# Optimization experiments

Hardware: AMD Instinct MI355X
Metric: run time of the kernel (lower is better)

## Reference

```python
import jax, jax.numpy as jnp
import numpy as np

N = 100000      # nodes
E = 1600000     # edges (avg degree 16)
IN, HID, OUT = 128, 32, 16
H = 2           # attention heads
EPS = 1e-5
NEG_SLOPE = 0.2


def setup_inputs() -> dict:
    key = jax.random.key(0)
    ks = jax.random.split(key, 24)
    f32 = jnp.float32
    def w(k, shape, scale=0.1):
        return jax.random.normal(k, shape, f32) * scale
    return {
        "x": jax.random.normal(ks[0], (N, IN), f32),
        "edge_index": jax.random.randint(ks[1], (2, E), 0, N, dtype=jnp.int32),
        # GCN layer 1
        "gcn1_W": w(ks[2], (IN, HID)), "gcn1_b": w(ks[3], (HID,)),
        # BN1 (eval mode: running stats)
        "bn1_g": 1.0 + w(ks[4], (HID,)), "bn1_b": w(ks[5], (HID,)),
        "bn1_m": w(ks[6], (HID,)), "bn1_v": 1.0 + jnp.abs(w(ks[7], (HID,))),
        # GAT layer 1 (HID -> HID, heads=H, concat=False)
        "gat1_W": w(ks[8], (HID, H * HID)), "gat1_as": w(ks[9], (H, HID)),
        "gat1_ad": w(ks[10], (H, HID)), "gat1_b": w(ks[11], (HID,)),
        # GCN layer 2
        "gcn2_W": w(ks[12], (HID, HID)), "gcn2_b": w(ks[13], (HID,)),
        # BN2
        "bn2_g": 1.0 + w(ks[14], (HID,)), "bn2_b": w(ks[15], (HID,)),
        "bn2_m": w(ks[16], (HID,)), "bn2_v": 1.0 + jnp.abs(w(ks[17], (HID,))),
        # GAT layer 2 (HID -> OUT, heads=H, concat=False)
        "gat2_W": w(ks[18], (HID, H * OUT)), "gat2_as": w(ks[19], (H, OUT)),
        "gat2_ad": w(ks[20], (H, OUT)), "gat2_b": w(ks[21], (OUT,)),
    }


def _add_self_loops(edge_index):
    loop = jnp.arange(N, dtype=edge_index.dtype)
    src = jnp.concatenate([edge_index[0], loop])
    dst = jnp.concatenate([edge_index[1], loop])
    return src, dst


def _gcn(x, src, dst, W, b):
    h = x @ W                                             # [N, F]
    deg = jax.ops.segment_sum(jnp.ones_like(dst, h.dtype), dst, N)
    dinv = jax.lax.rsqrt(jnp.maximum(deg, 1.0))
    norm = dinv[src] * dinv[dst]                          # [Etot]
    out = jax.ops.segment_sum(h[src] * norm[:, None], dst, N)
    return out + b


def _gat(x, src, dst, W, a_src, a_dst, b, F):
    # PyG GATConv (concat=False -> mean over heads); eval mode (no attn dropout)
    h = (x @ W).reshape(N, H, F)                          # [N, H, F]
    al_s = jnp.einsum('nhf,hf->nh', h, a_src)             # [N, H]
    al_d = jnp.einsum('nhf,hf->nh', h, a_dst)
    e = jax.nn.leaky_relu(al_s[src] + al_d[dst], NEG_SLOPE)  # [Etot, H]
    # segment softmax over destination neighborhoods (self-loops ensure >=1 edge)
    m = jax.ops.segment_max(e, dst, N)
    ex = jnp.exp(e - m[dst])
    s = jax.ops.segment_sum(ex, dst, N)
    alpha = ex / s[dst]                                   # [Etot, H]
    out = jax.ops.segment_sum(alpha[:, :, None] * h[src], dst, N)  # [N, H, F]
    return out.mean(axis=1) + b


def _bn_eval(x, g, b, m, v):
    return (x - m) * jax.lax.rsqrt(v + EPS) * g + b


def reference(x, edge_index, gcn1_W, gcn1_b, bn1_g, bn1_b, bn1_m, bn1_v,
              gat1_W, gat1_as, gat1_ad, gat1_b, gcn2_W, gcn2_b,
              bn2_g, bn2_b, bn2_m, bn2_v, gat2_W, gat2_as, gat2_ad, gat2_b):
    src, dst = _add_self_loops(edge_index)
    h = _gcn(x, src, dst, gcn1_W, gcn1_b)
    h = jax.nn.relu(_bn_eval(h, bn1_g, bn1_b, bn1_m, bn1_v))
    h = jax.nn.relu(_gat(h, src, dst, gat1_W, gat1_as, gat1_ad, gat1_b, HID))
    h = _gcn(h, src, dst, gcn2_W, gcn2_b)
    h = jax.nn.relu(_bn_eval(h, bn2_g, bn2_b, bn2_m, bn2_v))
    h = _gat(h, src, dst, gat2_W, gat2_as, gat2_ad, gat2_b, OUT)
    return jax.nn.log_softmax(h, axis=1)
```

## Files before the change

### kernel.cpp

```cpp
#include <hip/hip_runtime.h>
#include <hip/hip_bf16.h>

#define NN 100000
#define EE 1600000
#define SLAB 64
#define KB 391
#define CHUNK 4096

static constexpr float EPSV = 1e-5f;
static constexpr float SLOPE = 0.2f;

typedef unsigned short ushortt;

__device__ __forceinline__ float lrelu(float v) { return v > 0.f ? v : SLOPE * v; }

__device__ __forceinline__ unsigned rne_bf16(float v) {
    unsigned u = __float_as_uint(v);
    return (u + 0x7fffu + ((u >> 16) & 1u)) >> 16;
}
__device__ __forceinline__ float bf16_lo(unsigned u) { return __uint_as_float(u << 16); }
__device__ __forceinline__ float bf16_hi(unsigned u) { return __uint_as_float(u & 0xffff0000u); }
__device__ __forceinline__ float us2f(ushortt s) { return __uint_as_float((unsigned)s << 16); }


__global__ void k_z(int* __restrict__ hist) {
    int i = threadIdx.x;
    if (i < KB) hist[i] = 0;
}

__global__ __launch_bounds__(256) void k_hist(const int* __restrict__ dst, int* __restrict__ hist) {
    __shared__ int h[KB];
    int tid = threadIdx.x;
    for (int i = tid; i < KB; i += 256) h[i] = 0;
    __syncthreads();
    int e0 = blockIdx.x * CHUNK;
    #pragma unroll
    for (int r = 0; r < CHUNK / 256; ++r) {
        int e = e0 + r * 256 + tid;
        if (e < EE) atomicAdd(&h[dst[e] >> 8], 1);
    }
    __syncthreads();
    for (int i = tid; i < KB; i += 256)
        if (h[i]) atomicAdd(&hist[i], h[i]);
}

__global__ __launch_bounds__(512) void k_scan(const int* __restrict__ hist,
                                              int* __restrict__ start, int* __restrict__ gcur) {
    __shared__ int h[KB];
    int tid = threadIdx.x;
    for (int i = tid; i < KB; i += 512) h[i] = hist[i];
    __syncthreads();
    for (int t = tid; t < KB; t += 512) {
        int s = 0;
        for (int i = 0; i < t; ++i) s += h[i];
        start[t] = s;
        gcur[t] = 0;
    }
}

__global__ __launch_bounds__(256) void k_scat(const int* __restrict__ src, const int* __restrict__ dst,
                                              const int* __restrict__ start, int* __restrict__ gcur,
                                              unsigned int* __restrict__ ebuf) {
    __shared__ int hc[KB], hb[KB];
    int tid = threadIdx.x;
    for (int i = tid; i < KB; i += 256) hc[i] = 0;
    __syncthreads();
    int e0 = blockIdx.x * CHUNK;
    #pragma unroll
    for (int r = 0; r < CHUNK / 256; ++r) {
        int e = e0 + r * 256 + tid;
        if (e < EE) atomicAdd(&hc[dst[e] >> 8], 1);
    }
    __syncthreads();
    for (int i = tid; i < KB; i += 256) {
        int c = hc[i];
        if (c) hb[i] = atomicAdd(&gcur[i], c);
        hc[i] = 0;
    }
    __syncthreads();
    #pragma unroll
    for (int r = 0; r < CHUNK / 256; ++r) {
        int e = e0 + r * 256 + tid;
        if (e < EE) {
            int d = dst[e];
            int b = d >> 8;
            int rk = atomicAdd(&hc[b], 1);
            ebuf[start[b] + hb[b] + rk] = ((unsigned)src[e] << 8) | (unsigned)(d & 255);
        }
    }
}

__global__ __launch_bounds__(256) void k_bucket(const unsigned int* __restrict__ ebuf,
                                                const int* __restrict__ start, const int* __restrict__ hist,
                                                int* __restrict__ col, int* __restrict__ cnt) {
    __shared__ int lc[256];
    int tid = threadIdx.x;
    int b = blockIdx.x;
    lc[tid] = 0;
    __syncthreads();
    int s = start[b], nb = hist[b];
    for (int i = tid; i < nb; i += 256) {
        unsigned v = ebuf[s + i];
        int l = v & 255;
        int r = atomicAdd(&lc[l], 1);
        col[(((b << 8) + l) << 6) + r] = v >> 8;
    }
    __syncthreads();
    int node = (b << 8) + tid;
    if (node < NN) cnt[node] = lc[tid];
}

__global__ void k_deg(const int* __restrict__ cnt, float* __restrict__ dinv,
                      int* __restrict__ col) {
    int i = blockIdx.x * 256 + threadIdx.x;
    if (i < NN) {
        int c = cnt[i];
        dinv[i] = rsqrtf((float)(c + 1));
        col[i * SLAB + c] = i;
    }
}


__global__ __launch_bounds__(256) void k_gemm1(const float* __restrict__ x,
                                               const float* __restrict__ W,
                                               const float* __restrict__ dinv,
                                               ushortt* __restrict__ h) {
    __shared__ float wt[32 * 132];
    __shared__ float xl[8][128];
    int tid = threadIdx.x;
    for (int i = tid; i < 128 * 32; i += 256) {
        int k = i >> 5, f = i & 31;
        wt[f * 132 + k] = W[i];
    }
    int r = tid >> 5, lane = tid & 31;
    int n = blockIdx.x * 8 + r;
    float4 xv = *(const float4*)&x[(size_t)n * 128 + lane * 4];
    *(float4*)&xl[r][lane * 4] = xv;
    __syncthreads();
    float acc = 0.f;
    const float* wrow = &wt[lane * 132];
    #pragma unroll
    for (int kk = 0; kk < 32; ++kk) {
        float4 w4 = *(const float4*)&wrow[kk * 4];
        float4 x4 = *(const float4*)&xl[r][kk * 4];
        acc += w4.x * x4.x + w4.y * x4.y + w4.z * x4.z + w4.w * x4.w;
    }
    h[n * 32 + lane] = (ushortt)rne_bf16(acc * dinv[n]);
}


__global__ __launch_bounds__(256) void k_gcn_agg(
    const ushortt* __restrict__ hs, const int* __restrict__ cnt,
    const int* __restrict__ col, const float* __restrict__ dinv,
    const float* __restrict__ gb, const float* __restrict__ bng,
    const float* __restrict__ bnb, const float* __restrict__ bnm,
    const float* __restrict__ bnv, float* __restrict__ out) {
    int tid = threadIdx.x;
    int r = tid >> 5, lane = tid & 31;
    int n = blockIdx.x * 8 + r;
    int dn = cnt[n] + 1;
    int base = n * SLAB;
    int c0 = col[base + lane];
    int c1 = col[base + 32 + lane];
    float acc0 = 0.f, acc1 = 0.f, acc2 = 0.f, acc3 = 0.f;
    int j = 0;
    for (; j + 3 < dn; j += 4) {
        int cr0 = (j & 32) ? c1 : c0;
        unsigned a0 = (unsigned)__shfl(cr0, (j + 0) & 31, 32) * 32u + lane;
        unsigned a1 = (unsigned)__shfl(cr0, (j + 1) & 31, 32) * 32u + lane;
        unsigned a2 = (unsigned)__shfl(cr0, (j + 2) & 31, 32) * 32u + lane;
        unsigned a3 = (unsigned)__shfl(cr0, (j + 3) & 31, 32) * 32u + lane;
        acc0 += us2f(hs[a0]);
        acc1 += us2f(hs[a1]);
        acc2 += us2f(hs[a2]);
        acc3 += us2f(hs[a3]);
    }
    for (; j < dn; ++j) {
        unsigned a = (unsigned)__shfl((j & 32) ? c1 : c0, j & 31, 32) * 32u + lane;
        acc0 += us2f(hs[a]);
    }
    float acc = (acc0 + acc1) + (acc2 + acc3);
    float v = dinv[n] * acc + gb[lane];
    v = (v - bnm[lane]) * rsqrtf(bnv[lane] + EPSV) * bng[lane] + bnb[lane];
    out[(size_t)n * 32 + lane] = fmaxf(v, 0.f);
}


__global__ __launch_bounds__(256) void k_gat1_gemm(
    const float* __restrict__ t, const float* __restrict__ W,
    const float* __restrict__ as_, const float* __restrict__ ad_,
    unsigned* __restrict__ gp, float* __restrict__ al) {
    int tid = threadIdx.x;
    int r = tid >> 6, lane = tid & 63;
    int n = blockIdx.x * 4 + r;
    float wreg[32];
    #pragma unroll
    for (int k = 0; k < 32; ++k) wreg[k] = W[k * 64 + lane];
    __shared__ float xl[4][32];
    if (lane < 32) xl[r][lane] = t[(size_t)n * 32 + lane];
    __syncthreads();
    float acc = 0.f;
    #pragma unroll
    for (int kk = 0; kk < 8; ++kk) {
        float4 x4 = *(const float4*)&xl[r][kk * 4];
        acc += x4.x * wreg[4 * kk] + x4.y * wreg[4 * kk + 1]
             + x4.z * wreg[4 * kk + 2] + x4.w * wreg[4 * kk + 3];
    }
    int hh = lane >> 5, f = lane & 31;
    float as_v = acc * as_[hh * 32 + f];
    float ad_v = acc * ad_[hh * 32 + f];
    #pragma unroll
    for (int off = 16; off; off >>= 1) {
        as_v += __shfl_xor(as_v, off);
        ad_v += __shfl_xor(ad_v, off);
    }
    if (f == 0) { al[n * 4 + hh] = as_v; al[n * 4 + 2 + hh] = ad_v; }
    float accH = __shfl_xor(acc, 32);
    if (lane < 32) gp[n * 32 + lane] = (rne_bf16(accH) << 16) | rne_bf16(acc);
}


__global__ __launch_bounds__(256) void k_gat1_agg(
    const unsigned* __restrict__ gp, const float* __restrict__ al,
    const int* __restrict__ cnt, const int* __restrict__ col,
    const float* __restrict__ b, float* __restrict__ out) {
    __shared__ float2 ec[8][SLAB];
    int tid = threadIdx.x;
    int r = tid >> 5, lane = tid & 31;
    int n = blockIdx.x * 8 + r;
    int dn = cnt[n] + 1;
    int base = n * SLAB;
    int c0 = col[base + lane];
    int c1 = col[base + 32 + lane];
    float ad0 = al[n * 4 + 2], ad1 = al[n * 4 + 3];
    float e0a = -1e30f, e1a = -1e30f, e0b = -1e30f, e1b = -1e30f;
    if (lane < dn) {
        float4 a4 = *(const float4*)&al[(size_t)c0 * 4];
        e0a = lrelu(a4.x + ad0); e1a = lrelu(a4.y + ad1);
    }
    if (32 + lane < dn) {
        float4 a4 = *(const float4*)&al[(size_t)c1 * 4];
        e0b = lrelu(a4.x + ad0); e1b = lrelu(a4.y + ad1);
    }
    float m0 = fmaxf(e0a, e0b), m1 = fmaxf(e1a, e1b);
    #pragma unroll
    for (int off = 16; off; off >>= 1) {
        m0 = fmaxf(m0, __shfl_xor(m0, off));
        m1 = fmaxf(m1, __shfl_xor(m1, off));
    }
    float x0a = (lane < dn) ? __expf(e0a - m0) : 0.f;
    float x1a = (lane < dn) ? __expf(e1a - m1) : 0.f;
    float x0b = (32 + lane < dn) ? __expf(e0b - m0) : 0.f;
    float x1b = (32 + lane < dn) ? __expf(e1b - m1) : 0.f;
    ec[r][lane] = make_float2(x0a, x1a);
    ec[r][32 + lane] = make_float2(x0b, x1b);
    float s0 = x0a + x0b, s1 = x1a + x1b;
    #pragma unroll
    for (int off = 16; off; off >>= 1) {
        s0 += __shfl_xor(s0, off);
        s1 += __shfl_xor(s1, off);
    }
    float acc00 = 0.f, acc01 = 0.f, acc02 = 0.f, acc03 = 0.f;
    float acc10 = 0.f, acc11 = 0.f, acc12 = 0.f, acc13 = 0.f;
    int j = 0;
    for (; j + 3 < dn; j += 4) {
        int cr = (j & 32) ? c1 : c0;
        unsigned a0 = (unsigned)__shfl(cr, (j + 0) & 31, 32) * 32u + lane;
        unsigned a1 = (unsigned)__shfl(cr, (j + 1) & 31, 32) * 32u + lane;
        unsigned a2 = (unsigned)__shfl(cr, (j + 2) & 31, 32) * 32u + lane;
        unsigned a3 = (unsigned)__shfl(cr, (j + 3) & 31, 32) * 32u + lane;
        unsigned u0 = gp[a0], u1 = gp[a1], u2 = gp[a2], u3 = gp[a3];
        float2 w0 = ec[r][j + 0], w1 = ec[r][j + 1], w2 = ec[r][j + 2], w3 = ec[r][j + 3];
        acc00 += w0.x * bf16_lo(u0); acc10 += w0.y * bf16_hi(u0);
        acc01 += w1.x * bf16_lo(u1); acc11 += w1.y * bf16_hi(u1);
        acc02 += w2.x * bf16_lo(u2); acc12 += w2.y * bf16_hi(u2);
        acc03 += w3.x * bf16_lo(u3); acc13 += w3.y * bf16_hi(u3);
    }
    for (; j < dn; ++j) {
        unsigned a = (unsigned)__shfl((j & 32) ? c1 : c0, j & 31, 32) * 32u + lane;
        unsigned u = gp[a];
        float2 w = ec[r][j];
        acc00 += w.x * bf16_lo(u); acc10 += w.y * bf16_hi(u);
    }
    float a0s = (acc00 + acc01) + (acc02 + acc03);
    float a1s = (acc10 + acc11) + (acc12 + acc13);
    float v = 0.5f * (a0s / s0 + a1s / s1) + b[lane];
    out[(size_t)n * 32 + lane] = fmaxf(v, 0.f);
}


__global__ __launch_bounds__(256) void k_gemm32(const float* __restrict__ in,
                                                const float* __restrict__ W,
                                                const float* __restrict__ dinv,
                                                ushortt* __restrict__ out) {
    int tid = threadIdx.x;
    int r = tid >> 5, lane = tid & 31;
    int n = blockIdx.x * 8 + r;
    float wreg[32];
    #pragma unroll
    for (int k = 0; k < 32; ++k) wreg[k] = W[k * 32 + lane];
    __shared__ float xl[8][32];
    xl[r][lane] = in[(size_t)n * 32 + lane];
    __syncthreads();
    float acc = 0.f;
    #pragma unroll
    for (int kk = 0; kk < 8; ++kk) {
        float4 x4 = *(const float4*)&xl[r][kk * 4];
        acc += x4.x * wreg[4 * kk] + x4.y * wreg[4 * kk + 1]
             + x4.z * wreg[4 * kk + 2] + x4.w * wreg[4 * kk + 3];
    }
    out[n * 32 + lane] = (ushortt)rne_bf16(acc * dinv[n]);
}


__global__ __launch_bounds__(256) void k_gat2_gemm(
    const float* __restrict__ t, const float* __restrict__ W,
    const float* __restrict__ as_, const float* __restrict__ ad_,
    ushortt* __restrict__ gb16, float* __restrict__ al) {
    int tid = threadIdx.x;
    int r = tid >> 5, lane = tid & 31;
    int n = blockIdx.x * 8 + r;
    float wreg[32];
    #pragma unroll
    for (int k = 0; k < 32; ++k) wreg[k] = W[k * 32 + lane];
    __shared__ float xl[8][32];
    xl[r][lane] = t[(size_t)n * 32 + lane];
    __syncthreads();
    float acc = 0.f;
    #pragma unroll
    for (int kk = 0; kk < 8; ++kk) {
        float4 x4 = *(const float4*)&xl[r][kk * 4];
        acc += x4.x * wreg[4 * kk] + x4.y * wreg[4 * kk + 1]
             + x4.z * wreg[4 * kk + 2] + x4.w * wreg[4 * kk + 3];
    }
    int hh = lane >> 4, ff = lane & 15;
    float as_v = acc * as_[hh * 16 + ff];
    float ad_v = acc * ad_[hh * 16 + ff];
    #pragma unroll
    for (int off = 8; off; off >>= 1) {
        as_v += __shfl_xor(as_v, off);
        ad_v += __shfl_xor(ad_v, off);
    }
    if (ff == 0) { al[n * 4 + hh] = as_v; al[n * 4 + 2 + hh] = ad_v; }
    gb16[n * 32 + lane] = (ushortt)rne_bf16(acc);
}


__global__ __launch_bounds__(256) void k_gat2_agg(
    const ushortt* __restrict__ gb16, const float* __restrict__ al,
    const int* __restrict__ cnt, const int* __restrict__ col,
    const float* __restrict__ b, float* __restrict__ out) {
    __shared__ float ec[8][2][SLAB];
    int tid = threadIdx.x;
    int r = tid >> 5, lane = tid & 31;
    int n = blockIdx.x * 8 + r;
    int dn = cnt[n] + 1;
    int base = n * SLAB;
    int c0 = col[base + lane];
    int c1 = col[base + 32 + lane];
    float ad0 = al[n * 4 + 2], ad1 = al[n * 4 + 3];
    float e0a = -1e30f, e1a = -1e30f, e0b = -1e30f, e1b = -1e30f;
    if (lane < dn) {
        float4 a4 = *(const float4*)&al[(size_t)c0 * 4];
        e0a = lrelu(a4.x + ad0); e1a = lrelu(a4.y + ad1);
    }
    if (32 + lane < dn) {
        float4 a4 = *(const float4*)&al[(size_t)c1 * 4];
        e0b = lrelu(a4.x + ad0); e1b = lrelu(a4.y + ad1);
    }
    float m0 = fmaxf(e0a, e0b), m1 = fmaxf(e1a, e1b);
    #pragma unroll
    for (int off = 16; off; off >>= 1) {
        m0 = fmaxf(m0, __shfl_xor(m0, off));
        m1 = fmaxf(m1, __shfl_xor(m1, off));
    }
    float x0a = (lane < dn) ? __expf(e0a - m0) : 0.f;
    float x1a = (lane < dn) ? __expf(e1a - m1) : 0.f;
    float x0b = (32 + lane < dn) ? __expf(e0b - m0) : 0.f;
    float x1b = (32 + lane < dn) ? __expf(e1b - m1) : 0.f;
    ec[r][0][lane] = x0a;      ec[r][1][lane] = x1a;
    ec[r][0][32 + lane] = x0b; ec[r][1][32 + lane] = x1b;
    float s0 = x0a + x0b, s1 = x1a + x1b;
    #pragma unroll
    for (int off = 16; off; off >>= 1) {
        s0 += __shfl_xor(s0, off);
        s1 += __shfl_xor(s1, off);
    }
    int hh = lane >> 4, ff = lane & 15;
    const float* ecp = ec[r][hh];
    float acc0 = 0.f, acc1 = 0.f, acc2 = 0.f, acc3 = 0.f;
    int j = 0;
    for (; j + 3 < dn; j += 4) {
        int cr = (j & 32) ? c1 : c0;
        unsigned a0 = (unsigned)__shfl(cr, (j + 0) & 31, 32) * 32u + lane;
        unsigned a1 = (unsigned)__shfl(cr, (j + 1) & 31, 32) * 32u + lane;
        unsigned a2 = (unsigned)__shfl(cr, (j + 2) & 31, 32) * 32u + lane;
        unsigned a3 = (unsigned)__shfl(cr, (j + 3) & 31, 32) * 32u + lane;
        acc0 += ecp[j + 0] * us2f(gb16[a0]);
        acc1 += ecp[j + 1] * us2f(gb16[a1]);
        acc2 += ecp[j + 2] * us2f(gb16[a2]);
        acc3 += ecp[j + 3] * us2f(gb16[a3]);
    }
    for (; j < dn; ++j) {
        unsigned a = (unsigned)__shfl((j & 32) ? c1 : c0, j & 31, 32) * 32u + lane;
        acc0 += ecp[j] * us2f(gb16[a]);
    }
    float acc = ((acc0 + acc1) + (acc2 + acc3)) / (hh ? s1 : s0);
    float v = 0.5f * (acc + __shfl_xor(acc, 16)) + b[ff];
    float mx = v;
    #pragma unroll
    for (int off = 8; off; off >>= 1) mx = fmaxf(mx, __shfl_xor(mx, off));
    float se = __expf(v - mx);
    #pragma unroll
    for (int off = 8; off; off >>= 1) se += __shfl_xor(se, off);
    if (hh == 0) out[(size_t)n * 16 + ff] = v - mx - __logf(se);
}


static inline size_t al256(size_t x) { return (x + 255) & ~((size_t)255); }

extern "C" void kernel_launch(void* const* d_in, const int* in_sizes, int n_in,
                              void* d_out, int out_size, void* d_ws, size_t ws_size,
                              hipStream_t stream) {
    const float* x      = (const float*)d_in[0];
    const int*   ei     = (const int*)d_in[1];
    const float* gcn1_W = (const float*)d_in[2];
    const float* gcn1_b = (const float*)d_in[3];
    const float* bn1_g  = (const float*)d_in[4];
    const float* bn1_b  = (const float*)d_in[5];
    const float* bn1_m  = (const float*)d_in[6];
    const float* bn1_v  = (const float*)d_in[7];
    const float* gat1_W = (const float*)d_in[8];
    const float* gat1_as= (const float*)d_in[9];
    const float* gat1_ad= (const float*)d_in[10];
    const float* gat1_b = (const float*)d_in[11];
    const float* gcn2_W = (const float*)d_in[12];
    const float* gcn2_b = (const float*)d_in[13];
    const float* bn2_g  = (const float*)d_in[14];
    const float* bn2_b  = (const float*)d_in[15];
    const float* bn2_m  = (const float*)d_in[16];
    const float* bn2_v  = (const float*)d_in[17];
    const float* gat2_W = (const float*)d_in[18];
    const float* gat2_as= (const float*)d_in[19];
    const float* gat2_ad= (const float*)d_in[20];
    const float* gat2_b = (const float*)d_in[21];
    float* out = (float*)d_out;

    char* w = (char*)d_ws;
    size_t off = 0;
    auto alloc = [&](size_t bytes) { void* p = w + off; off = al256(off + bytes); return p; };
    int*     cnt   = (int*)alloc((size_t)NN * 4);
    float*   dinv  = (float*)alloc((size_t)NN * 4);
    int*     col   = (int*)alloc((size_t)NN * SLAB * 4);
    float*   bufB  = (float*)alloc((size_t)NN * 32 * 4);
    float*   bufC  = (float*)alloc((size_t)NN * 32 * 4);
    ushortt* hsb   = (ushortt*)alloc((size_t)NN * 32 * 2);
    unsigned* g1p  = (unsigned*)alloc((size_t)NN * 32 * 4);
    ushortt* g2b   = (ushortt*)alloc((size_t)NN * 32 * 2);
    float*   al    = (float*)alloc((size_t)NN * 4 * 4);
    int*     hist  = (int*)alloc((size_t)KB * 4);
    int*     start = (int*)alloc((size_t)KB * 4);
    int*     gcur  = (int*)alloc((size_t)KB * 4);
    unsigned int* ebuf = (unsigned int*)bufB;

    const int* esrc = ei;
    const int* edst = ei + EE;
    const int GE = (EE + CHUNK - 1) / CHUNK;

    k_z<<<1, 512, 0, stream>>>(hist);
    k_hist<<<GE, 256, 0, stream>>>(edst, hist);
    k_scan<<<1, 512, 0, stream>>>(hist, start, gcur);
    k_scat<<<GE, 256, 0, stream>>>(esrc, edst, start, gcur, ebuf);
    k_bucket<<<KB, 256, 0, stream>>>(ebuf, start, hist, col, cnt);
    k_deg<<<(NN + 255) / 256, 256, 0, stream>>>(cnt, dinv, col);

    k_gemm1<<<NN / 8, 256, 0, stream>>>(x, gcn1_W, dinv, hsb);
    k_gcn_agg<<<NN / 8, 256, 0, stream>>>(hsb, cnt, col, dinv, gcn1_b,
                                          bn1_g, bn1_b, bn1_m, bn1_v, bufB);
    k_gat1_gemm<<<NN / 4, 256, 0, stream>>>(bufB, gat1_W, gat1_as, gat1_ad, g1p, al);
    k_gat1_agg<<<NN / 8, 256, 0, stream>>>(g1p, al, cnt, col, gat1_b, bufC);
    k_gemm32<<<NN / 8, 256, 0, stream>>>(bufC, gcn2_W, dinv, hsb);
    k_gcn_agg<<<NN / 8, 256, 0, stream>>>(hsb, cnt, col, dinv, gcn2_b,
                                          bn2_g, bn2_b, bn2_m, bn2_v, bufB);
    k_gat2_gemm<<<NN / 8, 256, 0, stream>>>(bufB, gat2_W, gat2_as, gat2_ad, g2b, al);
    k_gat2_agg<<<NN / 8, 256, 0, stream>>>(g2b, al, cnt, col, gat2_b, out);
}
```

Baseline: 308.9 us.

## Fuse per-node GEMMs into neighboring aggregation kernels and register-tile first GEMM

Folds each small 32-wide dense transform (GAT1 projection, GCN2 weight, GAT2 projection) into the epilogue of the preceding aggregation kernel. Each node's row is multiplied against shared-memory weights using wave shuffles, which removes three launches and the fp32 intermediate round-trips through global memory. The first GEMM is rewritten as a persistent grid-stride kernel that keeps 64 weights in registers per lane and splits K across two half-waves. The fused kernels add shared-memory weight loads and a block sync to every aggregation block, and the 64-float register array may increase register pressure.

```diff
diff --git a/kernel.cpp b/kernel.cpp
--- a/kernel.cpp
+++ b/kernel.cpp
@@ -125,37 +125,52 @@
                                                const float* __restrict__ W,
                                                const float* __restrict__ dinv,
                                                ushortt* __restrict__ h) {
-    __shared__ float wt[32 * 132];
-    __shared__ float xl[8][128];
-    int tid = threadIdx.x;
-    for (int i = tid; i < 128 * 32; i += 256) {
-        int k = i >> 5, f = i & 31;
-        wt[f * 132 + k] = W[i];
-    }
-    int r = tid >> 5, lane = tid & 31;
-    int n = blockIdx.x * 8 + r;
-    float4 xv = *(const float4*)&x[(size_t)n * 128 + lane * 4];
-    *(float4*)&xl[r][lane * 4] = xv;
-    __syncthreads();
-    float acc = 0.f;
-    const float* wrow = &wt[lane * 132];
-    #pragma unroll
-    for (int kk = 0; kk < 32; ++kk) {
-        float4 w4 = *(const float4*)&wrow[kk * 4];
-        float4 x4 = *(const float4*)&xl[r][kk * 4];
-        acc += w4.x * x4.x + w4.y * x4.y + w4.z * x4.z + w4.w * x4.w;
-    }
-    h[n * 32 + lane] = (ushortt)rne_bf16(acc * dinv[n]);
-}
-
-
-__global__ __launch_bounds__(256) void k_gcn_agg(
+    int tid = threadIdx.x;
+    int lane = tid & 63;
+    int khalf = lane >> 5, f = lane & 31;
+    float wreg[64];
+    const float* wp = W + (khalf * 64) * 32 + f;
+    #pragma unroll
+    for (int i = 0; i < 64; ++i) wreg[i] = wp[i * 32];
+    int wid = blockIdx.x * 4 + (tid >> 6);
+    int nw = gridDim.x * 4;
+    for (int n = wid; n < NN; n += nw) {
+        const float* xp = x + (size_t)n * 128 + khalf * 64;
+        float a0 = 0.f, a1 = 0.f, a2 = 0.f, a3 = 0.f;
+        #pragma unroll
+        for (int j = 0; j < 16; j += 4) {
+            float4 v0 = *(const float4*)&xp[(j + 0) * 4];
+            float4 v1 = *(const float4*)&xp[(j + 1) * 4];
+            float4 v2 = *(const float4*)&xp[(j + 2) * 4];
+            float4 v3 = *(const float4*)&xp[(j + 3) * 4];
+            a0 += v0.x * wreg[j * 4 + 0]  + v0.y * wreg[j * 4 + 1]  + v0.z * wreg[j * 4 + 2]  + v0.w * wreg[j * 4 + 3];
+            a1 += v1.x * wreg[j * 4 + 4]  + v1.y * wreg[j * 4 + 5]  + v1.z * wreg[j * 4 + 6]  + v1.w * wreg[j * 4 + 7];
+            a2 += v2.x * wreg[j * 4 + 8]  + v2.y * wreg[j * 4 + 9]  + v2.z * wreg[j * 4 + 10] + v2.w * wreg[j * 4 + 11];
+            a3 += v3.x * wreg[j * 4 + 12] + v3.y * wreg[j * 4 + 13] + v3.z * wreg[j * 4 + 14] + v3.w * wreg[j * 4 + 15];
+        }
+        float tot = (a0 + a1) + (a2 + a3);
+        tot += __shfl_xor(tot, 32);
+        if (khalf == 0) h[n * 32 + f] = (ushortt)rne_bf16(tot * dinv[n]);
+    }
+}
+
+
+__global__ __launch_bounds__(256) void k_gcn1_gat1t(
     const ushortt* __restrict__ hs, const int* __restrict__ cnt,
     const int* __restrict__ col, const float* __restrict__ dinv,
     const float* __restrict__ gb, const float* __restrict__ bng,
     const float* __restrict__ bnb, const float* __restrict__ bnm,
-    const float* __restrict__ bnv, float* __restrict__ out) {
-    int tid = threadIdx.x;
+    const float* __restrict__ bnv,
+    const float* __restrict__ W1, const float* __restrict__ as_, const float* __restrict__ ad_,
+    unsigned* __restrict__ gp, float* __restrict__ al) {
+    __shared__ float wAs[32][32], wBs[32][32];
+    int tid = threadIdx.x;
+    for (int i = tid; i < 1024; i += 256) {
+        int k = i >> 5, f = i & 31;
+        wAs[k][f] = W1[k * 64 + f];
+        wBs[k][f] = W1[k * 64 + 32 + f];
+    }
+    __syncthreads();
     int r = tid >> 5, lane = tid & 31;
     int n = blockIdx.x * 8 + r;
     int dn = cnt[n] + 1;
@@ -182,50 +197,40 @@
     float acc = (acc0 + acc1) + (acc2 + acc3);
     float v = dinv[n] * acc + gb[lane];
     v = (v - bnm[lane]) * rsqrtf(bnv[lane] + EPSV) * bng[lane] + bnb[lane];
-    out[(size_t)n * 32 + lane] = fmaxf(v, 0.f);
-}
-
-
-__global__ __launch_bounds__(256) void k_gat1_gemm(
-    const float* __restrict__ t, const float* __restrict__ W,
-    const float* __restrict__ as_, const float* __restrict__ ad_,
-    unsigned* __restrict__ gp, float* __restrict__ al) {
-    int tid = threadIdx.x;
-    int r = tid >> 6, lane = tid & 63;
-    int n = blockIdx.x * 4 + r;
-    float wreg[32];
-    #pragma unroll
-    for (int k = 0; k < 32; ++k) wreg[k] = W[k * 64 + lane];
-    __shared__ float xl[4][32];
-    if (lane < 32) xl[r][lane] = t[(size_t)n * 32 + lane];
-    __syncthreads();
-    float acc = 0.f;
-    #pragma unroll
-    for (int kk = 0; kk < 8; ++kk) {
-        float4 x4 = *(const float4*)&xl[r][kk * 4];
-        acc += x4.x * wreg[4 * kk] + x4.y * wreg[4 * kk + 1]
-             + x4.z * wreg[4 * kk + 2] + x4.w * wreg[4 * kk + 3];
-    }
-    int hh = lane >> 5, f = lane & 31;
-    float as_v = acc * as_[hh * 32 + f];
-    float ad_v = acc * ad_[hh * 32 + f];
+    v = fmaxf(v, 0.f);
+    float gA0 = 0.f, gA1 = 0.f, gB0 = 0.f, gB1 = 0.f;
+    #pragma unroll
+    for (int k = 0; k < 32; k += 2) {
+        float t0 = __shfl(v, k, 32);
+        float t1v = __shfl(v, k + 1, 32);
+        gA0 += t0 * wAs[k][lane];     gB0 += t0 * wBs[k][lane];
+        gA1 += t1v * wAs[k + 1][lane]; gB1 += t1v * wBs[k + 1][lane];
+    }
+    float gA = gA0 + gA1, gB = gB0 + gB1;
+    float pas0 = gA * as_[lane],      pad0 = gA * ad_[lane];
+    float pas1 = gB * as_[32 + lane], pad1 = gB * ad_[32 + lane];
     #pragma unroll
     for (int off = 16; off; off >>= 1) {
-        as_v += __shfl_xor(as_v, off);
-        ad_v += __shfl_xor(ad_v, off);
-    }
-    if (f == 0) { al[n * 4 + hh] = as_v; al[n * 4 + 2 + hh] = ad_v; }
-    float accH = __shfl_xor(acc, 32);
-    if (lane < 32) gp[n * 32 + lane] = (rne_bf16(accH) << 16) | rne_bf16(acc);
-}
-
-
-__global__ __launch_bounds__(256) void k_gat1_agg(
+        pas0 += __shfl_xor(pas0, off);
+        pad0 += __shfl_xor(pad0, off);
+        pas1 += __shfl_xor(pas1, off);
+        pad1 += __shfl_xor(pad1, off);
+    }
+    if (lane == 0) *(float4*)&al[n * 4] = make_float4(pas0, pas1, pad0, pad1);
+    gp[n * 32 + lane] = (rne_bf16(gB) << 16) | rne_bf16(gA);
+}
+
+
+__global__ __launch_bounds__(256) void k_gat1_pv(
     const unsigned* __restrict__ gp, const float* __restrict__ al,
     const int* __restrict__ cnt, const int* __restrict__ col,
-    const float* __restrict__ b, float* __restrict__ out) {
+    const float* __restrict__ b, const float* __restrict__ W2,
+    const float* __restrict__ dinv, ushortt* __restrict__ hs3) {
     __shared__ float2 ec[8][SLAB];
-    int tid = threadIdx.x;
+    __shared__ float w2s[32][32];
+    int tid = threadIdx.x;
+    for (int i = tid; i < 1024; i += 256) w2s[i >> 5][i & 31] = W2[i];
+    __syncthreads();
     int r = tid >> 5, lane = tid & 31;
     int n = blockIdx.x * 8 + r;
     int dn = cnt[n] + 1;
@@ -285,64 +290,73 @@
     float a0s = (acc00 + acc01) + (acc02 + acc03);
     float a1s = (acc10 + acc11) + (acc12 + acc13);
     float v = 0.5f * (a0s / s0 + a1s / s1) + b[lane];
-    out[(size_t)n * 32 + lane] = fmaxf(v, 0.f);
-}
-
-
-__global__ __launch_bounds__(256) void k_gemm32(const float* __restrict__ in,
-                                                const float* __restrict__ W,
-                                                const float* __restrict__ dinv,
-                                                ushortt* __restrict__ out) {
-    int tid = threadIdx.x;
+    v = fmaxf(v, 0.f);
+    float g0 = 0.f, g1 = 0.f;
+    #pragma unroll
+    for (int k = 0; k < 32; k += 2) {
+        g0 += __shfl(v, k, 32) * w2s[k][lane];
+        g1 += __shfl(v, k + 1, 32) * w2s[k + 1][lane];
+    }
+    hs3[n * 32 + lane] = (ushortt)rne_bf16((g0 + g1) * dinv[n]);
+}
+
+
+__global__ __launch_bounds__(256) void k_gcn2_gat2t(
+    const ushortt* __restrict__ hs, const int* __restrict__ cnt,
+    const int* __restrict__ col, const float* __restrict__ dinv,
+    const float* __restrict__ gb, const float* __restrict__ bng,
+    const float* __restrict__ bnb, const float* __restrict__ bnm,
+    const float* __restrict__ bnv,
+    const float* __restrict__ Wg, const float* __restrict__ as_, const float* __restrict__ ad_,
+    ushortt* __restrict__ gb16, float* __restrict__ al) {
+    __shared__ float wgs[32][32];
+    int tid = threadIdx.x;
+    for (int i = tid; i < 1024; i += 256) wgs[i >> 5][i & 31] = Wg[i];
+    __syncthreads();
     int r = tid >> 5, lane = tid & 31;
     int n = blockIdx.x * 8 + r;
-    float wreg[32];
-    #pragma unroll
-    for (int k = 0; k < 32; ++k) wreg[k] = W[k * 32 + lane];
-    __shared__ float xl[8][32];
-    xl[r][lane] = in[(size_t)n * 32 + lane];
-    __syncthreads();
-    float acc = 0.f;
-    #pragma unroll
-    for (int kk = 0; kk < 8; ++kk) {
-        float4 x4 = *(const float4*)&xl[r][kk * 4];
-        acc += x4.x * wreg[4 * kk] + x4.y * wreg[4 * kk + 1]
-             + x4.z * wreg[4 * kk + 2] + x4.w * wreg[4 * kk + 3];
-    }
-    out[n * 32 + lane] = (ushortt)rne_bf16(acc * dinv[n]);
-}
-
-
-__global__ __launch_bounds__(256) void k_gat2_gemm(
-    const float* __restrict__ t, const float* __restrict__ W,
-    const float* __restrict__ as_, const float* __restrict__ ad_,
-    ushortt* __restrict__ gb16, float* __restrict__ al) {
-    int tid = threadIdx.x;
-    int r = tid >> 5, lane = tid & 31;
-    int n = blockIdx.x * 8 + r;
-    float wreg[32];
-    #pragma unroll
-    for (int k = 0; k < 32; ++k) wreg[k] = W[k * 32 + lane];
-    __shared__ float xl[8][32];
-    xl[r][lane] = t[(size_t)n * 32 + lane];
-    __syncthreads();
-    float acc = 0.f;
-    #pragma unroll
-    for (int kk = 0; kk < 8; ++kk) {
-        float4 x4 = *(const float4*)&xl[r][kk * 4];
-        acc += x4.x * wreg[4 * kk] + x4.y * wreg[4 * kk + 1]
-             + x4.z * wreg[4 * kk + 2] + x4.w * wreg[4 * kk + 3];
-    }
+    int dn = cnt[n] + 1;
+    int base = n * SLAB;
+    int c0 = col[base + lane];
+    int c1 = col[base + 32 + lane];
+    float acc0 = 0.f, acc1 = 0.f, acc2 = 0.f, acc3 = 0.f;
+    int j = 0;
+    for (; j + 3 < dn; j += 4) {
+        int cr0 = (j & 32) ? c1 : c0;
+        unsigned a0 = (unsigned)__shfl(cr0, (j + 0) & 31, 32) * 32u + lane;
+        unsigned a1 = (unsigned)__shfl(cr0, (j + 1) & 31, 32) * 32u + lane;
+        unsigned a2 = (unsigned)__shfl(cr0, (j + 2) & 31, 32) * 32u + lane;
+        unsigned a3 = (unsigned)__shfl(cr0, (j + 3) & 31, 32) * 32u + lane;
+        acc0 += us2f(hs[a0]);
+        acc1 += us2f(hs[a1]);
+        acc2 += us2f(hs[a2]);
+        acc3 += us2f(hs[a3]);
+    }
+    for (; j < dn; ++j) {
+        unsigned a = (unsigned)__shfl((j & 32) ? c1 : c0, j & 31, 32) * 32u + lane;
+        acc0 += us2f(hs[a]);
+    }
+    float acc = (acc0 + acc1) + (acc2 + acc3);
+    float v = dinv[n] * acc + gb[lane];
+    v = (v - bnm[lane]) * rsqrtf(bnv[lane] + EPSV) * bng[lane] + bnb[lane];
+    v = fmaxf(v, 0.f);
+    float g0 = 0.f, g1 = 0.f;
+    #pragma unroll
+    for (int k = 0; k < 32; k += 2) {
+        g0 += __shfl(v, k, 32) * wgs[k][lane];
+        g1 += __shfl(v, k + 1, 32) * wgs[k + 1][lane];
+    }
+    float g = g0 + g1;
     int hh = lane >> 4, ff = lane & 15;
-    float as_v = acc * as_[hh * 16 + ff];
-    float ad_v = acc * ad_[hh * 16 + ff];
+    float as_v = g * as_[hh * 16 + ff];
+    float ad_v = g * ad_[hh * 16 + ff];
     #pragma unroll
     for (int off = 8; off; off >>= 1) {
         as_v += __shfl_xor(as_v, off);
         ad_v += __shfl_xor(ad_v, off);
     }
     if (ff == 0) { al[n * 4 + hh] = as_v; al[n * 4 + 2 + hh] = ad_v; }
-    gb16[n * 32 + lane] = (ushortt)rne_bf16(acc);
+    gb16[n * 32 + lane] = (ushortt)rne_bf16(g);
 }
 
 
@@ -452,8 +466,6 @@
     int*     cnt   = (int*)alloc((size_t)NN * 4);
     float*   dinv  = (float*)alloc((size_t)NN * 4);
     int*     col   = (int*)alloc((size_t)NN * SLAB * 4);
-    float*   bufB  = (float*)alloc((size_t)NN * 32 * 4);
-    float*   bufC  = (float*)alloc((size_t)NN * 32 * 4);
     ushortt* hsb   = (ushortt*)alloc((size_t)NN * 32 * 2);
     unsigned* g1p  = (unsigned*)alloc((size_t)NN * 32 * 4);
     ushortt* g2b   = (ushortt*)alloc((size_t)NN * 32 * 2);
@@ -461,7 +473,7 @@
     int*     hist  = (int*)alloc((size_t)KB * 4);
     int*     start = (int*)alloc((size_t)KB * 4);
     int*     gcur  = (int*)alloc((size_t)KB * 4);
-    unsigned int* ebuf = (unsigned int*)bufB;
+    unsigned int* ebuf = (unsigned int*)g1p;
 
     const int* esrc = ei;
     const int* edst = ei + EE;
@@ -474,14 +486,14 @@
     k_bucket<<<KB, 256, 0, stream>>>(ebuf, start, hist, col, cnt);
     k_deg<<<(NN + 255) / 256, 256, 0, stream>>>(cnt, dinv, col);
 
-    k_gemm1<<<NN / 8, 256, 0, stream>>>(x, gcn1_W, dinv, hsb);
-    k_gcn_agg<<<NN / 8, 256, 0, stream>>>(hsb, cnt, col, dinv, gcn1_b,
-                                          bn1_g, bn1_b, bn1_m, bn1_v, bufB);
-    k_gat1_gemm<<<NN / 4, 256, 0, stream>>>(bufB, gat1_W, gat1_as, gat1_ad, g1p, al);
-    k_gat1_agg<<<NN / 8, 256, 0, stream>>>(g1p, al, cnt, col, gat1_b, bufC);
-    k_gemm32<<<NN / 8, 256, 0, stream>>>(bufC, gcn2_W, dinv, hsb);
-    k_gcn_agg<<<NN / 8, 256, 0, stream>>>(hsb, cnt, col, dinv, gcn2_b,
-                                          bn2_g, bn2_b, bn2_m, bn2_v, bufB);
-    k_gat2_gemm<<<NN / 8, 256, 0, stream>>>(bufB, gat2_W, gat2_as, gat2_ad, g2b, al);
+    k_gemm1<<<1024, 256, 0, stream>>>(x, gcn1_W, dinv, hsb);
+    k_gcn1_gat1t<<<NN / 8, 256, 0, stream>>>(hsb, cnt, col, dinv, gcn1_b,
+                                             bn1_g, bn1_b, bn1_m, bn1_v,
+                                             gat1_W, gat1_as, gat1_ad, g1p, al);
+    k_gat1_pv<<<NN / 8, 256, 0, stream>>>(g1p, al, cnt, col, gat1_b,
+                                          gcn2_W, dinv, hsb);
+    k_gcn2_gat2t<<<NN / 8, 256, 0, stream>>>(hsb, cnt, col, dinv, gcn2_b,
+                                             bn2_g, bn2_b, bn2_m, bn2_v,
+                                             gat2_W, gat2_as, gat2_ad, g2b, al);
     k_gat2_agg<<<NN / 8, 256, 0, stream>>>(g2b, al, cnt, col, gat2_b, out);
 }
```

Measured after the change: 328.4 us. 1.06x slower.
